# Performance work log

Hardware: AMD Instinct MI355X
Metric: run time of the kernel (lower is better)

The kernel has to match this reference:

```python
import jax, jax.numpy as jnp
import numpy as np

N_NODES = 50000
N_EDGES = 800000
IN_DIM = 128
HIDDEN = 128
N_GRAPHS = 64


def setup_inputs() -> dict:
    key = jax.random.key(0)
    ks = jax.random.split(key, 16)
    x = jax.random.normal(ks[0], (N_NODES, IN_DIM), dtype=jnp.float32)
    edge_index = jax.random.randint(ks[1], (2, N_EDGES), 0, N_NODES, dtype=jnp.int64)
    batch = jnp.sort(jax.random.randint(ks[2], (N_NODES,), 0, N_GRAPHS, dtype=jnp.int64))
    s = 1.0 / np.sqrt(IN_DIM)
    sh = 1.0 / np.sqrt(HIDDEN)
    return {
        "x": x,
        "edge_index": edge_index,
        "batch": batch,
        # SAGEConv1: lin_l (on aggregated neighbors, with bias), lin_r (on root, no bias)
        "w1l": jax.random.uniform(ks[3], (HIDDEN, IN_DIM), jnp.float32, -s, s),
        "b1l": jax.random.uniform(ks[4], (HIDDEN,), jnp.float32, -s, s),
        "w1r": jax.random.uniform(ks[5], (HIDDEN, IN_DIM), jnp.float32, -s, s),
        # SAGEConv2
        "w2l": jax.random.uniform(ks[6], (HIDDEN, HIDDEN), jnp.float32, -sh, sh),
        "b2l": jax.random.uniform(ks[7], (HIDDEN,), jnp.float32, -sh, sh),
        "w2r": jax.random.uniform(ks[8], (HIDDEN, HIDDEN), jnp.float32, -sh, sh),
        # MLP head
        "wl1": jax.random.uniform(ks[9], (64, HIDDEN), jnp.float32, -sh, sh),
        "bl1": jax.random.uniform(ks[10], (64,), jnp.float32, -sh, sh),
        "wout": jax.random.uniform(ks[11], (1, 64), jnp.float32, -0.125, 0.125),
        "bout": jax.random.uniform(ks[12], (1,), jnp.float32, -0.125, 0.125),
    }


def _sage_conv(x, src, dst, wl, bl, wr, n_nodes):
    # PyG SAGEConv (aggr='mean'): out = lin_l(mean_{j in N(i)} x_j) + lin_r(x_i)
    agg = jax.ops.segment_sum(x[src], dst, num_segments=n_nodes)  # [N, d]
    deg = jax.ops.segment_sum(jnp.ones_like(dst, dtype=x.dtype), dst, num_segments=n_nodes)
    agg = agg / jnp.maximum(deg, 1.0)[:, None]
    return agg @ wl.T + bl + x @ wr.T


def reference(x, edge_index, batch, w1l, b1l, w1r, w2l, b2l, w2r, wl1, bl1, wout, bout):
    src, dst = edge_index[0], edge_index[1]
    n = x.shape[0]
    h = jax.nn.relu(_sage_conv(x, src, dst, w1l, b1l, w1r, n))
    h = jax.nn.relu(_sage_conv(h, src, dst, w2l, b2l, w2r, n))
    # global_mean_pool over graph ids in `batch` -> [G, hidden]
    sums = jax.ops.segment_sum(h, batch, num_segments=N_GRAPHS)
    cnt = jax.ops.segment_sum(jnp.ones((n,), h.dtype), batch, num_segments=N_GRAPHS)
    g = sums / jnp.maximum(cnt, 1.0)[:, None]
    # MLP head (dropout is identity in eval mode)
    g = jax.nn.relu(g @ wl1.T + bl1)
    return jax.nn.sigmoid(g @ wout.T + bout)  # [G, 1]
```

## Files before the change

### kernel.cpp

```cpp
#include <hip/hip_runtime.h>
#include <cstdint>
#include <cstddef>

#define N_NODES  50000
#define N_EDGES  800000
#define DIM      128
#define N_GRAPHS 64
#define NB       196
#define BSH      8
#define EPB      2048
#define BPAD     16
#define CAP      8192
#define NBB      391
#define NPREP    1579

typedef __attribute__((ext_vector_type(8))) short     bf16x8;
typedef __attribute__((ext_vector_type(4))) float     f32x4;

__device__ __forceinline__ int clamp_node(int v) {
    return v < 0 ? 0 : (v >= N_NODES ? N_NODES - 1 : v);
}
__device__ __forceinline__ unsigned short f2bf(float f) {
    union { float f; unsigned u; } v; v.f = f;
    unsigned r = v.u + 0x7FFF + ((v.u >> 16) & 1);
    return (unsigned short)(r >> 16);
}
__device__ __forceinline__ float bflo(unsigned u) {
    union { unsigned u; float f; } v; v.u = u << 16; return v.f;
}
__device__ __forceinline__ float bfhi(unsigned u) {
    union { unsigned u; float f; } v; v.u = u & 0xFFFF0000u; return v.f;
}

__global__ __launch_bounds__(512) void k_front(const int* __restrict__ ei,
                                               int* __restrict__ bcur,
                                               unsigned* __restrict__ tmp,
                                               const float* __restrict__ x,
                                               unsigned short* __restrict__ xb,
                                               const float* __restrict__ W1l,
                                               const float* __restrict__ W1r,
                                               const float* __restrict__ W2l,
                                               const float* __restrict__ W2r,
                                               unsigned short* __restrict__ wbuf1,
                                               unsigned short* __restrict__ wbuf2) {
    int t = threadIdx.x;

    if (blockIdx.x >= NBB) {
        int i = (blockIdx.x - NBB) * 512 + t;
        const int n8 = N_NODES * 16;
        if (i < n8) {
            const float4* p = (const float4*)(x + (size_t)i * 8);
            float4 a = p[0], b = p[1];
            union { unsigned short s[8]; uint4 u; } o;
            o.s[0] = f2bf(a.x); o.s[1] = f2bf(a.y); o.s[2] = f2bf(a.z); o.s[3] = f2bf(a.w);
            o.s[4] = f2bf(b.x); o.s[5] = f2bf(b.y); o.s[6] = f2bf(b.z); o.s[7] = f2bf(b.w);
            *(uint4*)(xb + (size_t)i * 8) = o.u;
            return;
        }
        int tid = i - n8;
        if (tid >= 2 * 8 * 8 * 64) return;
        int which = tid >> 12;
        int id    = tid & 4095;
        const float* Wl = which ? W2l : W1l;
        const float* Wr = which ? W2r : W1r;
        unsigned short* wbuf = which ? wbuf2 : wbuf1;
        int lane = id & 63;
        int ks   = (id >> 6) & 7;
        int ot   = id >> 9;
        int o  = ot * 16 + (lane & 15);
        int kb = ks * 32 + ((lane >> 4) << 3);
        union { unsigned short s[8]; uint4 u; } frag;
        #pragma unroll
        for (int j = 0; j < 8; ++j) {
            int k = kb + j;
            float v = (k < DIM) ? Wl[o * DIM + k] : Wr[o * DIM + (k - DIM)];
            frag.s[j] = f2bf(v);
        }
        *(uint4*)(wbuf + (size_t)id * 8) = frag.u;
        return;
    }

    __shared__ int cnt[256], cur[256], ofs[256];
    __shared__ int s[512];
    __shared__ unsigned list[EPB];
    int base = blockIdx.x * EPB;
    int eend = base + EPB; if (eend > N_EDGES) eend = N_EDGES;

    if (t < 256) cnt[t] = 0;
    __syncthreads();

    int d[4], sv[4];
    bool ok[4];
    #pragma unroll
    for (int i = 0; i < 4; ++i) {
        int e = base + t + i * 512;
        ok[i] = (e < eend);
        if (ok[i]) {
            d[i]  = clamp_node(ei[N_EDGES + e]);
            sv[i] = clamp_node(ei[e]);
            atomicAdd(&cnt[d[i] >> BSH], 1);
        }
    }
    __syncthreads();
    int v = (t < 256) ? cnt[t] : 0;
    s[t] = v;
    __syncthreads();
    for (int off = 1; off < 256; off <<= 1) {
        int y = (t >= off && t < 256) ? s[t - off] : 0;
        __syncthreads();
        if (t < 256) s[t] += y;
        __syncthreads();
    }
    if (t < 256) { ofs[t] = s[t] - v; cur[t] = s[t] - v; }
    __syncthreads();
    #pragma unroll
    for (int i = 0; i < 4; ++i) {
        if (ok[i]) {
            int b = d[i] >> BSH;
            int p = atomicAdd(&cur[b], 1);
            list[p] = (unsigned)sv[i] | ((unsigned)(d[i] & 255) << 16);
        }
    }
    __syncthreads();
    int wv = t >> 6, lane = t & 63;
    const int NGRP = 25;
    for (int jj = 0; jj < NGRP; ++jj) {
        int b = wv + 8 * ((jj + (int)blockIdx.x) % NGRP);
        if (b >= NB) continue;
        int c = cnt[b];
        if (c == 0) continue;
        int gpos;
        if (lane == 0) gpos = atomicAdd(&bcur[b * BPAD], c);
        gpos = __shfl(gpos, 0);
        if (gpos + c > CAP) c = (gpos < CAP) ? (CAP - gpos) : 0;
        int ls = ofs[b];
        for (int i = lane; i < c; i += 64) tmp[b * CAP + gpos + i] = list[ls + i];
    }
}

__global__ __launch_bounds__(512) void k_csr(const unsigned* __restrict__ tmp,
                                             const int* __restrict__ bcur,
                                             int2* __restrict__ rsse,
                                             int* __restrict__ srcs,
                                             float* __restrict__ gsum) {
    __shared__ int lh[256], lcur[256];
    __shared__ int s[512];
    int b = blockIdx.x;
    int t = threadIdx.x;
    int base = b * CAP;
    int nc = bcur[b * BPAD];
    if (nc > CAP) nc = CAP;

    int gi = b * 512 + t;
    if (gi < N_GRAPHS * DIM) gsum[gi] = 0.f;

    if (t < 256) lh[t] = 0;
    __syncthreads();
    for (int e = t; e < nc; e += 512)
        atomicAdd(&lh[tmp[base + e] >> 16], 1);
    __syncthreads();
    int v = (t < 256) ? lh[t] : 0;
    s[t] = v;
    __syncthreads();
    for (int off = 1; off < 256; off <<= 1) {
        int y = (t >= off && t < 256) ? s[t - off] : 0;
        __syncthreads();
        if (t < 256) s[t] += y;
        __syncthreads();
    }
    if (t < 256) {
        int st = s[t] - v;
        lcur[t] = st;
        int node = (b << BSH) + t;
        if (node < N_NODES) rsse[node] = make_int2(base + st, base + st + v);
    }
    __syncthreads();
    for (int e = t; e < nc; e += 512) {
        unsigned val = tmp[base + e];
        int pos = atomicAdd(&lcur[val >> 16], 1);
        srcs[base + pos] = (int)(val & 0xFFFFu);
    }
}

__global__ __launch_bounds__(256) void k_sage(const unsigned short* __restrict__ feat,
                                              const unsigned short* __restrict__ in2b,
                                              const int2* __restrict__ rsse,
                                              const int* __restrict__ srcs,
                                              const unsigned short* __restrict__ wbuf,
                                              const float* __restrict__ bias,
                                              unsigned short* __restrict__ outb) {
    __shared__ unsigned short almp[16][136];
    int t    = threadIdx.x;
    int wave = t >> 6;
    int lane = t & 63;
    int n0   = blockIdx.x * 16;

    {
        int q   = lane >> 4;
        int sub = lane & 15;
        int node  = n0 + wave * 4 + q;
        int2 se   = rsse[node];
        int start = se.x;
        int end   = se.y;
        float a0 = 0.f, a1 = 0.f, a2 = 0.f, a3 = 0.f;
        float a4 = 0.f, a5 = 0.f, a6 = 0.f, a7 = 0.f;
        const size_t coff = (size_t)sub * 8;

#define ACC8(r) { a0 += bflo(r.x); a1 += bfhi(r.x); a2 += bflo(r.y); a3 += bfhi(r.y); \
                  a4 += bflo(r.z); a5 += bfhi(r.z); a6 += bflo(r.w); a7 += bfhi(r.w); }
        int e = start;
        for (; e + 12 <= end; e += 12) {
            int s0 = srcs[e + 0], s1 = srcs[e + 1], s2 = srcs[e + 2];
            int s3 = srcs[e + 3], s4 = srcs[e + 4], s5 = srcs[e + 5];
            int s6 = srcs[e + 6], s7 = srcs[e + 7], s8 = srcs[e + 8];
            int s9 = srcs[e + 9], s10 = srcs[e + 10], s11 = srcs[e + 11];
            uint4 r0  = *(const uint4*)(feat + (size_t)s0  * DIM + coff);
            uint4 r1  = *(const uint4*)(feat + (size_t)s1  * DIM + coff);
            uint4 r2  = *(const uint4*)(feat + (size_t)s2  * DIM + coff);
            uint4 r3  = *(const uint4*)(feat + (size_t)s3  * DIM + coff);
            uint4 r4  = *(const uint4*)(feat + (size_t)s4  * DIM + coff);
            uint4 r5  = *(const uint4*)(feat + (size_t)s5  * DIM + coff);
            uint4 r6  = *(const uint4*)(feat + (size_t)s6  * DIM + coff);
            uint4 r7  = *(const uint4*)(feat + (size_t)s7  * DIM + coff);
            uint4 r8  = *(const uint4*)(feat + (size_t)s8  * DIM + coff);
            uint4 r9  = *(const uint4*)(feat + (size_t)s9  * DIM + coff);
            uint4 r10 = *(const uint4*)(feat + (size_t)s10 * DIM + coff);
            uint4 r11 = *(const uint4*)(feat + (size_t)s11 * DIM + coff);
            ACC8(r0) ACC8(r1) ACC8(r2) ACC8(r3) ACC8(r4) ACC8(r5)
            ACC8(r6) ACC8(r7) ACC8(r8) ACC8(r9) ACC8(r10) ACC8(r11)
        }
        for (; e + 4 <= end; e += 4) {
            uint4 r0 = *(const uint4*)(feat + (size_t)srcs[e + 0] * DIM + coff);
            uint4 r1 = *(const uint4*)(feat + (size_t)srcs[e + 1] * DIM + coff);
            uint4 r2 = *(const uint4*)(feat + (size_t)srcs[e + 2] * DIM + coff);
            uint4 r3 = *(const uint4*)(feat + (size_t)srcs[e + 3] * DIM + coff);
            ACC8(r0) ACC8(r1) ACC8(r2) ACC8(r3)
        }
        for (; e < end; ++e) {
            uint4 r0 = *(const uint4*)(feat + (size_t)srcs[e] * DIM + coff);
            ACC8(r0)
        }
#undef ACC8
        float inv = 1.0f / fmaxf((float)(end - start), 1.0f);
        union { unsigned short s[8]; uint4 u; } o;
        o.s[0] = f2bf(a0 * inv); o.s[1] = f2bf(a1 * inv);
        o.s[2] = f2bf(a2 * inv); o.s[3] = f2bf(a3 * inv);
        o.s[4] = f2bf(a4 * inv); o.s[5] = f2bf(a5 * inv);
        o.s[6] = f2bf(a6 * inv); o.s[7] = f2bf(a7 * inv);
        *(uint4*)&almp[wave * 4 + q][sub * 8] = o.u;
    }
    __syncthreads();

    int row = lane & 15;
    int kl  = (lane >> 4) << 3;
    bf16x8 A[8];
    #pragma unroll
    for (int ks = 0; ks < 4; ++ks)
        A[ks] = *(const bf16x8*)&almp[row][kl + ks * 32];
    const unsigned short* xrow = in2b + (size_t)(n0 + row) * DIM + kl;
    #pragma unroll
    for (int ks = 0; ks < 4; ++ks)
        A[4 + ks] = *(const bf16x8*)(xrow + ks * 32);

    const unsigned short* wb0 = wbuf + ((size_t)(wave * 2)     * 8 * 64 + lane) * 8;
    const unsigned short* wb1 = wbuf + ((size_t)(wave * 2 + 1) * 8 * 64 + lane) * 8;
    f32x4 acc0 = {0.f, 0.f, 0.f, 0.f}, acc1 = {0.f, 0.f, 0.f, 0.f};
    #pragma unroll
    for (int ks = 0; ks < 8; ++ks) {
        bf16x8 b0 = *(const bf16x8*)(wb0 + (size_t)ks * 64 * 8);
        bf16x8 b1 = *(const bf16x8*)(wb1 + (size_t)ks * 64 * 8);
        acc0 = __builtin_amdgcn_mfma_f32_16x16x32_bf16(A[ks], b0, acc0, 0, 0, 0);
        acc1 = __builtin_amdgcn_mfma_f32_16x16x32_bf16(A[ks], b1, acc1, 0, 0, 0);
    }

    int o0   = wave * 32;
    int ocol = lane & 15;
    int rb   = (lane >> 4) << 2;
    float b0 = bias[o0 + ocol];
    float b1 = bias[o0 + 16 + ocol];
    #pragma unroll
    for (int r = 0; r < 4; ++r) {
        size_t n = (size_t)(n0 + rb + r);
        outb[n * DIM + o0 + ocol]      = f2bf(fmaxf(acc0[r] + b0, 0.f));
        outb[n * DIM + o0 + 16 + ocol] = f2bf(fmaxf(acc1[r] + b1, 0.f));
    }
}

__global__ __launch_bounds__(256) void k_pool_partial(const unsigned short* __restrict__ h2,
                                                      const int* __restrict__ batch,
                                                      float* __restrict__ gsum) {
    int wid  = (blockIdx.x * 256 + threadIdx.x) >> 6;
    int lane = threadIdx.x & 63;
    int n0 = wid * 32;
    if (n0 >= N_NODES) return;
    int n1 = n0 + 32; if (n1 > N_NODES) n1 = N_NODES;
    int col = lane * 2;

    float ax = 0.f, ay = 0.f;
    int cur = batch[n0];
    for (int n = n0; n < n1; ++n) {
        int b = batch[n];
        if (b != cur) {
            atomicAdd(&gsum[cur * DIM + col], ax);
            atomicAdd(&gsum[cur * DIM + col + 1], ay);
            ax = 0.f; ay = 0.f; cur = b;
        }
        unsigned u = *(const unsigned*)(h2 + (size_t)n * DIM + col);
        ax += bflo(u); ay += bfhi(u);
    }
    atomicAdd(&gsum[cur * DIM + col], ax);
    atomicAdd(&gsum[cur * DIM + col + 1], ay);
}

__global__ __launch_bounds__(256) void k_head(const float* __restrict__ gsum,
                                              const int* __restrict__ batch,
                                              const float* __restrict__ wl1,
                                              const float* __restrict__ bl1,
                                              const float* __restrict__ wout,
                                              const float* __restrict__ bout,
                                              float* __restrict__ out) {
    int g = blockIdx.x;
    int t = threadIdx.x;

    int lo = 0, hi = N_NODES;
    while (lo < hi) { int mid = (lo + hi) >> 1; if (batch[mid] < g) lo = mid + 1; else hi = mid; }
    int s = lo;
    lo = 0; hi = N_NODES;
    while (lo < hi) { int mid = (lo + hi) >> 1; if (batch[mid] < g + 1) lo = mid + 1; else hi = mid; }
    int e = lo;

    __shared__ float gvec[DIM];
    if (t < DIM) {
        float cnt = fmaxf((float)(e - s), 1.0f);
        gvec[t] = gsum[g * DIM + t] / cnt;
    }
    __syncthreads();
    if (t < 64) {
        float a = bl1[t];
        #pragma unroll 4
        for (int k = 0; k < DIM; ++k) a += wl1[t * DIM + k] * gvec[k];
        float g1 = fmaxf(a, 0.f) * wout[t];
        #pragma unroll
        for (int off = 32; off > 0; off >>= 1) g1 += __shfl_down(g1, off);
        if (t == 0) {
            float z = g1 + bout[0];
            out[g] = 1.0f / (1.0f + expf(-z));
        }
    }
}

extern "C" void kernel_launch(void* const* d_in, const int* in_sizes, int n_in,
                              void* d_out, int out_size, void* d_ws, size_t ws_size,
                              hipStream_t stream) {
    const float* x     = (const float*)d_in[0];
    const int*   ei    = (const int*)d_in[1];
    const int*   batch = (const int*)d_in[2];
    const float* w1l   = (const float*)d_in[3];
    const float* b1l   = (const float*)d_in[4];
    const float* w1r   = (const float*)d_in[5];
    const float* w2l   = (const float*)d_in[6];
    const float* b2l   = (const float*)d_in[7];
    const float* w2r   = (const float*)d_in[8];
    const float* wl1   = (const float*)d_in[9];
    const float* bl1   = (const float*)d_in[10];
    const float* wout  = (const float*)d_in[11];
    const float* bout  = (const float*)d_in[12];
    float* out = (float*)d_out;

    char*  wsp = (char*)d_ws;
    size_t off = 0;
    auto alloc = [&](size_t bytes) -> char* {
        char* p = wsp + off;
        off += (bytes + 255) & ~(size_t)255;
        return p;
    };
    int*  bcur = (int*)alloc((size_t)NB * BPAD * 4);
    int2* rsse = (int2*)alloc((size_t)N_NODES * 8);
    int*  srcs = (int*)alloc((size_t)NB * CAP * 4);
    unsigned* tmp = (unsigned*)alloc((size_t)NB * CAP * 4);
    unsigned short* xb    = (unsigned short*)alloc((size_t)N_NODES * DIM * 2);
    unsigned short* h1b   = (unsigned short*)alloc((size_t)N_NODES * DIM * 2);
    unsigned short* h2b   = (unsigned short*)alloc((size_t)N_NODES * DIM * 2);
    unsigned short* wbuf1 = (unsigned short*)alloc((size_t)8 * 8 * 64 * 8 * 2);
    unsigned short* wbuf2 = (unsigned short*)alloc((size_t)8 * 8 * 64 * 8 * 2);
    float* gsum = (float*)alloc((size_t)N_GRAPHS * DIM * 4);

    hipMemsetAsync(bcur, 0, (size_t)NB * BPAD * 4, stream);

    k_front<<<NBB + NPREP, 512, 0, stream>>>(ei, bcur, tmp, x, xb,
                                             w1l, w1r, w2l, w2r, wbuf1, wbuf2);
    k_csr<<<NB, 512, 0, stream>>>(tmp, bcur, rsse, srcs, gsum);

    k_sage<<<N_NODES / 16, 256, 0, stream>>>(xb, xb, rsse, srcs, wbuf1, b1l, h1b);
    k_sage<<<N_NODES / 16, 256, 0, stream>>>(h1b, h1b, rsse, srcs, wbuf2, b2l, h2b);
    k_pool_partial<<<(N_NODES + 127) / 128, 256, 0, stream>>>(h2b, batch, gsum);
    k_head<<<N_GRAPHS, 256, 0, stream>>>(gsum, batch, wl1, bl1, wout, bout, out);
}
```

Baseline: 149.4 us.

## Fuse global mean pooling into second SAGE layer epilogue

The second SAGE layer's epilogue now accumulates ReLU outputs directly into per-graph sums with atomics instead of writing h2 to memory and running a separate pooling kernel. When all 16 nodes in a block share one graph, values are reduced across the wave with shuffles before one atomic per column. Otherwise each row issues its own atomic. This removes one kernel launch and the h2 write/read traffic, but adds atomic contention on gsum and changes fp32 summation order.

```diff
diff --git a/kernel.cpp b/kernel.cpp
--- a/kernel.cpp
+++ b/kernel.cpp
@@ -182,18 +182,24 @@
     }
 }
 
+template<int POOL>
 __global__ __launch_bounds__(256) void k_sage(const unsigned short* __restrict__ feat,
                                               const unsigned short* __restrict__ in2b,
                                               const int2* __restrict__ rsse,
                                               const int* __restrict__ srcs,
                                               const unsigned short* __restrict__ wbuf,
                                               const float* __restrict__ bias,
-                                              unsigned short* __restrict__ outb) {
+                                              unsigned short* __restrict__ outb,
+                                              const int* __restrict__ batch,
+                                              float* __restrict__ gsum) {
     __shared__ unsigned short almp[16][136];
+    __shared__ int sb[16];
     int t    = threadIdx.x;
     int wave = t >> 6;
     int lane = t & 63;
     int n0   = blockIdx.x * 16;
+
+    if (POOL && t < 16) sb[t] = batch[n0 + t];
 
     {
         int q   = lane >> 4;
@@ -278,38 +284,40 @@
     int rb   = (lane >> 4) << 2;
     float b0 = bias[o0 + ocol];
     float b1 = bias[o0 + 16 + ocol];
-    #pragma unroll
-    for (int r = 0; r < 4; ++r) {
-        size_t n = (size_t)(n0 + rb + r);
-        outb[n * DIM + o0 + ocol]      = f2bf(fmaxf(acc0[r] + b0, 0.f));
-        outb[n * DIM + o0 + 16 + ocol] = f2bf(fmaxf(acc1[r] + b1, 0.f));
-    }
-}
-
-__global__ __launch_bounds__(256) void k_pool_partial(const unsigned short* __restrict__ h2,
-                                                      const int* __restrict__ batch,
-                                                      float* __restrict__ gsum) {
-    int wid  = (blockIdx.x * 256 + threadIdx.x) >> 6;
-    int lane = threadIdx.x & 63;
-    int n0 = wid * 32;
-    if (n0 >= N_NODES) return;
-    int n1 = n0 + 32; if (n1 > N_NODES) n1 = N_NODES;
-    int col = lane * 2;
-
-    float ax = 0.f, ay = 0.f;
-    int cur = batch[n0];
-    for (int n = n0; n < n1; ++n) {
-        int b = batch[n];
-        if (b != cur) {
-            atomicAdd(&gsum[cur * DIM + col], ax);
-            atomicAdd(&gsum[cur * DIM + col + 1], ay);
-            ax = 0.f; ay = 0.f; cur = b;
-        }
-        unsigned u = *(const unsigned*)(h2 + (size_t)n * DIM + col);
-        ax += bflo(u); ay += bfhi(u);
-    }
-    atomicAdd(&gsum[cur * DIM + col], ax);
-    atomicAdd(&gsum[cur * DIM + col + 1], ay);
+
+    if (POOL) {
+        float v0[4], v1[4];
+        #pragma unroll
+        for (int r = 0; r < 4; ++r) {
+            v0[r] = fmaxf(acc0[r] + b0, 0.f);
+            v1[r] = fmaxf(acc1[r] + b1, 0.f);
+        }
+        int g0 = sb[0], g15 = sb[15];
+        if (g0 == g15) {
+            float s0 = v0[0] + v0[1] + v0[2] + v0[3];
+            float s1 = v1[0] + v1[1] + v1[2] + v1[3];
+            s0 += __shfl_xor(s0, 16); s0 += __shfl_xor(s0, 32);
+            s1 += __shfl_xor(s1, 16); s1 += __shfl_xor(s1, 32);
+            if (lane < 16) {
+                atomicAdd(&gsum[g0 * DIM + o0 + ocol], s0);
+                atomicAdd(&gsum[g0 * DIM + o0 + 16 + ocol], s1);
+            }
+        } else {
+            #pragma unroll
+            for (int r = 0; r < 4; ++r) {
+                int g = sb[rb + r];
+                atomicAdd(&gsum[g * DIM + o0 + ocol], v0[r]);
+                atomicAdd(&gsum[g * DIM + o0 + 16 + ocol], v1[r]);
+            }
+        }
+    } else {
+        #pragma unroll
+        for (int r = 0; r < 4; ++r) {
+            size_t n = (size_t)(n0 + rb + r);
+            outb[n * DIM + o0 + ocol]      = f2bf(fmaxf(acc0[r] + b0, 0.f));
+            outb[n * DIM + o0 + 16 + ocol] = f2bf(fmaxf(acc1[r] + b1, 0.f));
+        }
+    }
 }
 
 __global__ __launch_bounds__(256) void k_head(const float* __restrict__ gsum,
@@ -380,7 +388,6 @@
     unsigned* tmp = (unsigned*)alloc((size_t)NB * CAP * 4);
     unsigned short* xb    = (unsigned short*)alloc((size_t)N_NODES * DIM * 2);
     unsigned short* h1b   = (unsigned short*)alloc((size_t)N_NODES * DIM * 2);
-    unsigned short* h2b   = (unsigned short*)alloc((size_t)N_NODES * DIM * 2);
     unsigned short* wbuf1 = (unsigned short*)alloc((size_t)8 * 8 * 64 * 8 * 2);
     unsigned short* wbuf2 = (unsigned short*)alloc((size_t)8 * 8 * 64 * 8 * 2);
     float* gsum = (float*)alloc((size_t)N_GRAPHS * DIM * 4);
@@ -391,8 +398,9 @@
                                              w1l, w1r, w2l, w2r, wbuf1, wbuf2);
     k_csr<<<NB, 512, 0, stream>>>(tmp, bcur, rsse, srcs, gsum);
 
-    k_sage<<<N_NODES / 16, 256, 0, stream>>>(xb, xb, rsse, srcs, wbuf1, b1l, h1b);
-    k_sage<<<N_NODES / 16, 256, 0, stream>>>(h1b, h1b, rsse, srcs, wbuf2, b2l, h2b);
-    k_pool_partial<<<(N_NODES + 127) / 128, 256, 0, stream>>>(h2b, batch, gsum);
+    k_sage<0><<<N_NODES / 16, 256, 0, stream>>>(xb, xb, rsse, srcs, wbuf1, b1l,
+                                                h1b, batch, gsum);
+    k_sage<1><<<N_NODES / 16, 256, 0, stream>>>(h1b, h1b, rsse, srcs, wbuf2, b2l,
+                                                nullptr, batch, gsum);
     k_head<<<N_GRAPHS, 256, 0, stream>>>(gsum, batch, wl1, bl1, wout, bout, out);
 }
```

After: 135.1 us. 9.6% less time.
